# Kernel optimization log

Measured on AMD Instinct MI355X. Metric: run time of the kernel, lower is better.

Reference implementation:

```python
import jax, jax.numpy as jnp
import numpy as np

N_NODES = 100000


def _gcn_conv(x, src, dst, W, b, n):
    # PyG GCNConv: x' = D^-1/2 (A + I) D^-1/2 (x W) + b, edges flow src -> dst
    h = x @ W                                        # [n, out]
    ones = jnp.ones(src.shape[0], dtype=h.dtype)
    deg = jax.ops.segment_sum(ones, dst, num_segments=n) + 1.0  # +1 for self-loop
    dis = jax.lax.rsqrt(deg)                         # deg >= 1, no inf handling needed
    norm = dis[src] * dis[dst]                       # [E]
    agg = jax.ops.segment_sum(norm[:, None] * h[src], dst, num_segments=n)
    agg = agg + (dis * dis)[:, None] * h             # self-loop term, norm_ii = 1/deg_i
    return agg + b


def setup_inputs() -> dict:
    key = jax.random.key(0)
    k1, k2, k3, k4, k5, k6, k7, k8 = jax.random.split(key, 8)
    in_c, hid = 128, 64
    x = jax.random.normal(k1, (N_NODES, in_c), dtype=jnp.float32)
    edge_index = jax.random.randint(k2, (2, 1600000), 0, N_NODES, dtype=jnp.int64)
    s1 = 1.0 / np.sqrt(in_c)
    s2 = 1.0 / np.sqrt(hid)
    W1 = jax.random.uniform(k3, (in_c, hid), jnp.float32, -s1, s1)
    b1 = jnp.zeros((hid,), jnp.float32)
    W2 = jax.random.uniform(k4, (hid, hid), jnp.float32, -s2, s2)
    b2 = jnp.zeros((hid,), jnp.float32)
    Wl = jax.random.uniform(k5, (hid, 1), jnp.float32, -s2, s2)
    bl = jax.random.uniform(k6, (1,), jnp.float32, -s2, s2)
    return {"x": x, "edge_index": edge_index, "W1": W1, "b1": b1,
            "W2": W2, "b2": b2, "Wl": Wl, "bl": bl}


def reference(x, edge_index, W1, b1, W2, b2, Wl, bl):
    src, dst = edge_index[0], edge_index[1]
    n = x.shape[0]
    h = jax.nn.relu(_gcn_conv(x, src, dst, W1, b1, n))
    # dropout is identity in eval mode
    h = _gcn_conv(h, src, dst, W2, b2, n)
    return jax.nn.sigmoid(h @ Wl + bl)               # [n, 1]
```

## Files before the change

### kernel.cpp

```cpp
#include <hip/hip_runtime.h>
#include <hip/hip_bf16.h>


#define EPB 4096
#define NBMAX 512

typedef __attribute__((ext_vector_type(8))) short bf16x8;
typedef __attribute__((ext_vector_type(4))) float f32x4;

__device__ __forceinline__ unsigned short f2b(float f) {
    unsigned u = __builtin_bit_cast(unsigned, f);
    u += 0x7fffu + ((u >> 16) & 1u);
    return (unsigned short)(u >> 16);
}
__device__ __forceinline__ float b2f(unsigned short h) {
    unsigned u = (unsigned)h << 16;
    return __builtin_bit_cast(float, u);
}


__global__ __launch_bounds__(256) void bcount_k(
    const int* __restrict__ dst, int* __restrict__ bucket_cnt, int E, int nbuckets) {
    __shared__ int lh[NBMAX];
    int t = threadIdx.x;
    for (int i = t; i < nbuckets; i += 256) lh[i] = 0;
    __syncthreads();
    int e0 = blockIdx.x * EPB;
    int cnt = min(EPB, E - e0);
    for (int i = t; i < cnt; i += 256) atomicAdd(&lh[dst[e0 + i] >> 8], 1);
    __syncthreads();
    for (int i = t; i < nbuckets; i += 256)
        if (lh[i]) atomicAdd(&bucket_cnt[i], lh[i]);
}

__global__ __launch_bounds__(512) void bscan_k(
    const int* __restrict__ cnt, int* __restrict__ base, int* __restrict__ cur, int nb) {
    __shared__ int s[512];
    int t = threadIdx.x;
    int v = (t < nb) ? cnt[t] : 0;
    s[t] = v; __syncthreads();
    #pragma unroll
    for (int off = 1; off < 512; off <<= 1) {
        int u = (t >= off) ? s[t - off] : 0;
        __syncthreads();
        s[t] += u;
        __syncthreads();
    }
    if (t < nb) { int e = s[t] - v; base[t] = e; cur[t] = e; }
    if (t == nb - 1) base[nb] = s[t];
}

__global__ __launch_bounds__(256) void partition_k(
    const int* __restrict__ src, const int* __restrict__ dst,
    int* __restrict__ bucket_cur, int* __restrict__ stage, int E, int nbuckets) {
    __shared__ int ls[EPB];
    __shared__ int ld[EPB];
    __shared__ int lhist[NBMAX];
    __shared__ int lbase[NBMAX];
    int e0 = blockIdx.x * EPB;
    int cnt = min(EPB, E - e0);
    int t = threadIdx.x;
    for (int i = t; i < cnt; i += 256) { ls[i] = src[e0 + i]; ld[i] = dst[e0 + i]; }
    for (int b = t; b < nbuckets; b += 256) lhist[b] = 0;
    __syncthreads();
    for (int i = t; i < cnt; i += 256) atomicAdd(&lhist[ld[i] >> 8], 1);
    __syncthreads();
    for (int b = t; b < nbuckets; b += 256) {
        int c = lhist[b];
        lbase[b] = (c > 0) ? atomicAdd(&bucket_cur[b], c) : 0;
        lhist[b] = 0;
    }
    __syncthreads();
    for (int i = t; i < cnt; i += 256) {
        int d  = ld[i];
        int b  = d >> 8;
        int off = atomicAdd(&lhist[b], 1);
        stage[lbase[b] + off] = ls[i] | ((d & 255) << 17);
    }
}

__global__ __launch_bounds__(256) void bucket_place_k(
    const int* __restrict__ stage, const int* __restrict__ bucket_base,
    int* __restrict__ row_start, float* __restrict__ dis,
    int* __restrict__ csr_src, int n, int nbuckets) {
    __shared__ int lh[256];
    __shared__ int ss[256];
    __shared__ int lcur[256];
    int b = blockIdx.x;
    int t = threadIdx.x;
    int ebeg = bucket_base[b], eend = bucket_base[b + 1];
    int node0 = b << 8;

    lh[t] = 0;
    __syncthreads();
    for (int e = ebeg + t; e < eend; e += 256)
        atomicAdd(&lh[(stage[e] >> 17) & 255], 1);
    __syncthreads();

    int cnt = lh[t];
    ss[t] = cnt;
    __syncthreads();
    #pragma unroll
    for (int off = 1; off < 256; off <<= 1) {
        int u = (t >= off) ? ss[t - off] : 0;
        __syncthreads();
        ss[t] += u;
        __syncthreads();
    }
    int excl = ss[t] - cnt;
    int node = node0 + t;
    if (node < n) {
        row_start[node] = ebeg + excl;
        dis[node] = rsqrtf((float)cnt + 1.0f);
    }
    lcur[t] = ebeg + excl;
    if (b == nbuckets - 1 && t == 0) row_start[n] = eend;
    __syncthreads();

    for (int e = ebeg + t; e < eend; e += 256) {
        int p = stage[e];
        int pos = atomicAdd(&lcur[(p >> 17) & 255], 1);
        csr_src[pos] = p & 0x1FFFF;
    }
}

__global__ void wfrag_k(const float* __restrict__ W1, const float* __restrict__ W2,
                        unsigned short* __restrict__ fw1, float* __restrict__ w2l,
                        const float* __restrict__ b2, const float* __restrict__ Wl,
                        const float* __restrict__ bl, float* __restrict__ c0,
                        int* __restrict__ bcnt) {
    int gid = blockIdx.x * blockDim.x + threadIdx.x;
    if (gid <= NBMAX) bcnt[gid] = 0;
    if (blockIdx.x == 0 && threadIdx.x < 64) {
        float v = b2[threadIdx.x] * Wl[threadIdx.x];
        #pragma unroll
        for (int m = 32; m >= 1; m >>= 1) v += __shfl_xor(v, m);
        if (threadIdx.x == 0) c0[0] = v + bl[0];
    }
    if (blockIdx.x == 1 && threadIdx.x < 64) {
        int k = threadIdx.x;
        float s = 0.f;
        #pragma unroll 8
        for (int j = 0; j < 64; ++j) s = fmaf(W2[k * 64 + j], Wl[j], s);
        w2l[k] = s;
    }
    if (gid < 8192) {
        int f = gid >> 9, rem = gid & 511;
        int l = rem >> 3, i = rem & 7;
        int ks = f >> 2, ct = f & 3;
        int k = ks * 32 + ((l >> 4) << 3) + i;
        int c = ct * 16 + (l & 15);
        fw1[gid] = f2b(W1[k * 64 + c]);
    }
}

template <int K>
__global__ __launch_bounds__(256) void mfma_gemm_k(
    const float* __restrict__ X, const unsigned short* __restrict__ FW,
    const float* __restrict__ dis, unsigned short* __restrict__ Y, int n) {
    constexpr int KS = K / 32;
    int wave   = (int)((blockIdx.x * blockDim.x + threadIdx.x) >> 6);
    int lane   = threadIdx.x & 63;
    int nwaves = (int)((gridDim.x * blockDim.x) >> 6);
    int ntiles = n >> 4;

    bf16x8 bfrag[KS][4];
    #pragma unroll
    for (int ks = 0; ks < KS; ++ks)
        #pragma unroll
        for (int ct = 0; ct < 4; ++ct)
            bfrag[ks][ct] = *reinterpret_cast<const bf16x8*>(FW + ((ks * 4 + ct) << 9) + (lane << 3));

    int rb = lane & 15;
    int kb = (lane >> 4) << 3;

    for (int tile = wave; tile < ntiles; tile += nwaves) {
        int row = (tile << 4) + rb;
        f32x4 acc[4];
        #pragma unroll
        for (int ct = 0; ct < 4; ++ct) acc[ct] = (f32x4){0.f, 0.f, 0.f, 0.f};

        #pragma unroll
        for (int ks = 0; ks < KS; ++ks) {
            const float* p = X + (size_t)row * K + ks * 32 + kb;
            float4 u = *reinterpret_cast<const float4*>(p);
            float4 v = *reinterpret_cast<const float4*>(p + 4);
            bf16x8 af;
            af[0] = (short)f2b(u.x); af[1] = (short)f2b(u.y);
            af[2] = (short)f2b(u.z); af[3] = (short)f2b(u.w);
            af[4] = (short)f2b(v.x); af[5] = (short)f2b(v.y);
            af[6] = (short)f2b(v.z); af[7] = (short)f2b(v.w);
            #pragma unroll
            for (int ct = 0; ct < 4; ++ct)
                acc[ct] = __builtin_amdgcn_mfma_f32_16x16x32_bf16(af, bfrag[ks][ct], acc[ct], 0, 0, 0);
        }

        int orow0 = (tile << 4) + ((lane >> 4) << 2);
        int ocol  = lane & 15;
        float dv0 = dis[orow0], dv1 = dis[orow0 + 1], dv2 = dis[orow0 + 2], dv3 = dis[orow0 + 3];
        #pragma unroll
        for (int ct = 0; ct < 4; ++ct) {
            Y[(size_t)(orow0 + 0) * 64 + ct * 16 + ocol] = f2b(acc[ct][0] * dv0);
            Y[(size_t)(orow0 + 1) * 64 + ct * 16 + ocol] = f2b(acc[ct][1] * dv1);
            Y[(size_t)(orow0 + 2) * 64 + ct * 16 + ocol] = f2b(acc[ct][2] * dv2);
            Y[(size_t)(orow0 + 3) * 64 + ct * 16 + ocol] = f2b(acc[ct][3] * dv3);
        }
    }
}

__global__ __launch_bounds__(256) void gather_k(
    const int* __restrict__ row_start, const int* __restrict__ csr_src,
    const float* __restrict__ dis, const unsigned short* __restrict__ tp,
    const float* __restrict__ b, const float* __restrict__ w2l,
    float* __restrict__ z, int n) {
    int node = (int)((blockIdx.x * blockDim.x + threadIdx.x) >> 6);
    int lane = threadIdx.x & 63;
    if (node >= n) return;
    int beg = row_start[node], end = row_start[node + 1];
    float dd = dis[node];
    float a0 = b2f(tp[(size_t)node * 64 + lane]);
    float a1 = 0.f, a2 = 0.f, a3 = 0.f, a4 = 0.f, a5 = 0.f, a6 = 0.f, a7 = 0.f;

    for (int base = beg; base < end; base += 64) {
        int rem = end - base;
        int cnt = rem < 64 ? rem : 64;
        int idx = (lane < cnt) ? csr_src[base + lane] : 0;
        int j = 0;
        for (; j + 8 <= cnt; j += 8) {
            int s0 = __shfl(idx, j + 0), s1 = __shfl(idx, j + 1);
            int s2 = __shfl(idx, j + 2), s3 = __shfl(idx, j + 3);
            int s4 = __shfl(idx, j + 4), s5 = __shfl(idx, j + 5);
            int s6 = __shfl(idx, j + 6), s7 = __shfl(idx, j + 7);
            a0 += b2f(tp[(size_t)s0 * 64 + lane]);
            a1 += b2f(tp[(size_t)s1 * 64 + lane]);
            a2 += b2f(tp[(size_t)s2 * 64 + lane]);
            a3 += b2f(tp[(size_t)s3 * 64 + lane]);
            a4 += b2f(tp[(size_t)s4 * 64 + lane]);
            a5 += b2f(tp[(size_t)s5 * 64 + lane]);
            a6 += b2f(tp[(size_t)s6 * 64 + lane]);
            a7 += b2f(tp[(size_t)s7 * 64 + lane]);
        }
        if (j + 4 <= cnt) {
            int s0 = __shfl(idx, j + 0), s1 = __shfl(idx, j + 1);
            int s2 = __shfl(idx, j + 2), s3 = __shfl(idx, j + 3);
            a0 += b2f(tp[(size_t)s0 * 64 + lane]);
            a1 += b2f(tp[(size_t)s1 * 64 + lane]);
            a2 += b2f(tp[(size_t)s2 * 64 + lane]);
            a3 += b2f(tp[(size_t)s3 * 64 + lane]);
            j += 4;
        }
        for (; j < cnt; ++j) {
            int s = __shfl(idx, j);
            a4 += b2f(tp[(size_t)s * 64 + lane]);
        }
    }

    float acc = ((a0 + a1) + (a2 + a3)) + ((a4 + a5) + (a6 + a7));
    float h = fmaxf(fmaf(dd, acc, b[lane]), 0.f);
    float v = h * w2l[lane];
    #pragma unroll
    for (int m = 32; m >= 1; m >>= 1) v += __shfl_xor(v, m);
    if (lane == 0) z[node] = dd * v;
}

__global__ __launch_bounds__(256) void gatherz_k(
    const int* __restrict__ row_start, const int* __restrict__ csr_src,
    const float* __restrict__ dis, const float* __restrict__ z,
    const float* __restrict__ c0, float* __restrict__ out, int n) {
    int i = blockIdx.x * blockDim.x + threadIdx.x;
    if (i >= n) return;
    int beg = row_start[i], end = row_start[i + 1];
    float s0 = 0.f, s1 = 0.f, s2 = 0.f, s3 = 0.f;
    int e = beg;
    for (; e + 4 <= end; e += 4) {
        s0 += z[csr_src[e + 0]];
        s1 += z[csr_src[e + 1]];
        s2 += z[csr_src[e + 2]];
        s3 += z[csr_src[e + 3]];
    }
    for (; e < end; ++e) s0 += z[csr_src[e]];
    float v = fmaf(dis[i], z[i] + ((s0 + s1) + (s2 + s3)), c0[0]);
    out[i] = 1.f / (1.f + expf(-v));
}


__global__ void relu_k(float* __restrict__ p, long long m) {
    long long i = (long long)blockIdx.x * blockDim.x + threadIdx.x;
    if (i < m) p[i] = fmaxf(p[i], 0.f);
}
__global__ void deg_init_k(float* __restrict__ deg, int n) {
    int i = blockIdx.x * blockDim.x + threadIdx.x;
    if (i < n) deg[i] = 1.0f;
}
__global__ void deg_edges_k(const int* __restrict__ dst, float* __restrict__ deg, int E) {
    int e = blockIdx.x * blockDim.x + threadIdx.x;
    if (e < E) atomicAdd(&deg[dst[e]], 1.0f);
}
__global__ void dis_k(float* __restrict__ deg, int n) {
    int i = blockIdx.x * blockDim.x + threadIdx.x;
    if (i < n) deg[i] = rsqrtf(deg[i]);
}
__global__ void init_agg_k(const float* __restrict__ t, const float* __restrict__ dis,
                           const float* __restrict__ b, float* __restrict__ agg, int n) {
    int idx = blockIdx.x * blockDim.x + threadIdx.x;
    if (idx >= n * 64) return;
    int i = idx >> 6, jj = idx & 63;
    float ds = dis[i];
    agg[idx] = ds * ds * t[idx] + b[jj];
}
__global__ __launch_bounds__(256) void agg_edges_k(
    const int* __restrict__ src, const int* __restrict__ dst,
    const float* __restrict__ dis, const float* __restrict__ t,
    float* __restrict__ agg, int E) {
    int e    = (int)((blockIdx.x * blockDim.x + threadIdx.x) >> 6);
    int lane = threadIdx.x & 63;
    if (e >= E) return;
    int s = src[e], d = dst[e];
    float w = dis[s] * dis[d];
    atomicAdd(&agg[(size_t)d * 64 + lane], w * t[(size_t)s * 64 + lane]);
}
__global__ __launch_bounds__(256) void final_k(
    const float* __restrict__ agg, const float* __restrict__ Wl,
    const float* __restrict__ bl, float* __restrict__ out, int n) {
    int node = (int)((blockIdx.x * blockDim.x + threadIdx.x) >> 6);
    int lane = threadIdx.x & 63;
    if (node >= n) return;
    float v = agg[(size_t)node * 64 + lane] * Wl[lane];
    #pragma unroll
    for (int m = 32; m >= 1; m >>= 1) v += __shfl_xor(v, m);
    if (lane == 0) out[node] = 1.f / (1.f + expf(-(v + bl[0])));
}
template <int K>
__global__ __launch_bounds__(256) void gemm_rows4_k(
    const float* __restrict__ X, const float* __restrict__ W,
    float* __restrict__ Y, int n) {
    __shared__ float Ws[K * 64];
    for (int t = threadIdx.x; t < K * 64; t += blockDim.x) Ws[t] = W[t];
    __syncthreads();
    int wave   = (int)((blockIdx.x * blockDim.x + threadIdx.x) >> 6);
    int lane   = threadIdx.x & 63;
    int nwaves = (int)((gridDim.x * blockDim.x) >> 6);
    for (int r = wave; r < n; r += nwaves) {
        const float* xr = X + (size_t)r * K;
        float acc = 0.f;
        for (int k = 0; k < K; k += 4) {
            float4 a = *reinterpret_cast<const float4*>(xr + k);
            acc = fmaf(a.x, Ws[(k + 0) * 64 + lane], acc);
            acc = fmaf(a.y, Ws[(k + 1) * 64 + lane], acc);
            acc = fmaf(a.z, Ws[(k + 2) * 64 + lane], acc);
            acc = fmaf(a.w, Ws[(k + 3) * 64 + lane], acc);
        }
        Y[(size_t)r * 64 + lane] = acc;
    }
}


extern "C" void kernel_launch(void* const* d_in, const int* in_sizes, int n_in,
                              void* d_out, int out_size, void* d_ws, size_t ws_size,
                              hipStream_t stream) {
    const float* x  = (const float*)d_in[0];
    const int*   ei = (const int*)d_in[1];
    const float* W1 = (const float*)d_in[2];
    const float* b1 = (const float*)d_in[3];
    const float* W2 = (const float*)d_in[4];
    const float* b2 = (const float*)d_in[5];
    const float* Wl = (const float*)d_in[6];
    const float* bl = (const float*)d_in[7];
    float* out = (float*)d_out;

    const int n = in_sizes[0] / 128;
    const int E = in_sizes[1] / 2;
    const int* src = ei;
    const int* dst = ei + E;

    const int B = 256;
    dim3 blk(B);
    auto align512 = [](size_t v) { return (v + 511) & ~(size_t)511; };

    char* ws = (char*)d_ws;
    size_t off = 0;
    float*          dis     = (float*)(ws + off); off = align512(off + (size_t)n * 4);
    int*            row_st  = (int*)  (ws + off); off = align512(off + (size_t)(n + 1) * 4);
    int*            bcnt    = (int*)  (ws + off); off = align512(off + (size_t)(NBMAX + 1) * 4);
    int*            bbase   = (int*)  (ws + off); off = align512(off + (size_t)(NBMAX + 1) * 4);
    int*            bcur    = (int*)  (ws + off); off = align512(off + (size_t)NBMAX * 4);
    float*          c0      = (float*)(ws + off); off = align512(off + 512);
    float*          w2l     = (float*)(ws + off); off = align512(off + 64 * 4);
    float*          zbuf    = (float*)(ws + off); off = align512(off + (size_t)n * 4);
    int*            csr_src = (int*)  (ws + off); off = align512(off + (size_t)E * 4);
    unsigned short* bufA16  = (unsigned short*)(ws + off); off = align512(off + (size_t)n * 64 * 2);
    int*            stage   = (int*)  (ws + off); off = align512(off + (size_t)E * 4);
    unsigned short* fw1     = (unsigned short*)(ws + off); off = align512(off + 8192 * 2);
    size_t need_csr = off;

    const int nbuckets = (n + 255) >> 8;
    const int nebl = (E + EPB - 1) / EPB;

    if (ws_size >= need_csr && (n & 15) == 0 && nbuckets <= NBMAX && n <= (1 << 17)) {
        wfrag_k<<<48, blk, 0, stream>>>(W1, W2, fw1, w2l, b2, Wl, bl, c0, bcnt);

        bcount_k<<<nebl, blk, 0, stream>>>(dst, bcnt, E, nbuckets);
        bscan_k<<<1, 512, 0, stream>>>(bcnt, bbase, bcur, nbuckets);
        partition_k<<<nebl, blk, 0, stream>>>(src, dst, bcur, stage, E, nbuckets);
        bucket_place_k<<<nbuckets, blk, 0, stream>>>(stage, bbase, row_st, dis, csr_src, n, nbuckets);

        int gemm_blocks = ((n >> 4) + 3) / 4;

        mfma_gemm_k<128><<<gemm_blocks, blk, 0, stream>>>(x, fw1, dis, bufA16, n);

        gather_k<<<((size_t)n * 64 + B - 1) / B, blk, 0, stream>>>(
            row_st, csr_src, dis, bufA16, b1, w2l, zbuf, n);

        gatherz_k<<<(n + B - 1) / B, blk, 0, stream>>>(
            row_st, csr_src, dis, zbuf, c0, out, n);
    } else {
        size_t o2 = 0;
        float* dis2 = (float*)(ws + o2); o2 = align512(o2 + (size_t)n * 4);
        float* bA   = (float*)(ws + o2); o2 += (size_t)n * 64 * 4;
        float* bB   = (float*)(ws + o2);

        deg_init_k<<<(n + B - 1) / B, blk, 0, stream>>>(dis2, n);
        deg_edges_k<<<(E + B - 1) / B, blk, 0, stream>>>(dst, dis2, E);
        dis_k<<<(n + B - 1) / B, blk, 0, stream>>>(dis2, n);

        gemm_rows4_k<128><<<2048, blk, 0, stream>>>(x, W1, bA, n);
        init_agg_k<<<((size_t)n * 64 + B - 1) / B, blk, 0, stream>>>(bA, dis2, b1, bB, n);
        agg_edges_k<<<(E + 3) / 4, blk, 0, stream>>>(src, dst, dis2, bA, bB, E);
        relu_k<<<((size_t)n * 64 + B - 1) / B, blk, 0, stream>>>(bB, (long long)n * 64);

        gemm_rows4_k<64><<<2048, blk, 0, stream>>>(bB, W2, bA, n);
        init_agg_k<<<((size_t)n * 64 + B - 1) / B, blk, 0, stream>>>(bA, dis2, b2, bB, n);
        agg_edges_k<<<(E + 3) / 4, blk, 0, stream>>>(src, dst, dis2, bA, bB, E);

        final_k<<<(n + 3) / 4, blk, 0, stream>>>(bB, Wl, bl, out, n);
    }
}
```

Before: 132.6 us.

## Split gather features into four column-partitioned passes with per-pass partial sums

The GEMM now writes its bf16 output in four column-major slabs of 16 features, each of size n×16. The gather kernel launches four passes, one slab per pass, so each pass's working set is a quarter of the full feature table and is more likely to stay in cache. Within a wave, 8 edges are processed at once with each lane loading a 32-bit pair of features. Per-pass partial z values are written to a buffer and combined by a new zsum kernel. This adds an extra launch, four passes over the CSR index data, and cross-lane shuffle reductions.

```diff
diff --git a/kernel.cpp b/kernel.cpp
--- a/kernel.cpp
+++ b/kernel.cpp
@@ -16,6 +16,12 @@
 __device__ __forceinline__ float b2f(unsigned short h) {
     unsigned u = (unsigned)h << 16;
     return __builtin_bit_cast(float, u);
+}
+__device__ __forceinline__ float blo(unsigned u) {
+    return __builtin_bit_cast(float, u << 16);
+}
+__device__ __forceinline__ float bhi(unsigned u) {
+    return __builtin_bit_cast(float, u & 0xffff0000u);
 }
 
 
@@ -163,6 +169,7 @@
     int lane   = threadIdx.x & 63;
     int nwaves = (int)((gridDim.x * blockDim.x) >> 6);
     int ntiles = n >> 4;
+    size_t n16 = (size_t)n * 16;
 
     bf16x8 bfrag[KS][4];
     #pragma unroll
@@ -200,10 +207,11 @@
         float dv0 = dis[orow0], dv1 = dis[orow0 + 1], dv2 = dis[orow0 + 2], dv3 = dis[orow0 + 3];
         #pragma unroll
         for (int ct = 0; ct < 4; ++ct) {
-            Y[(size_t)(orow0 + 0) * 64 + ct * 16 + ocol] = f2b(acc[ct][0] * dv0);
-            Y[(size_t)(orow0 + 1) * 64 + ct * 16 + ocol] = f2b(acc[ct][1] * dv1);
-            Y[(size_t)(orow0 + 2) * 64 + ct * 16 + ocol] = f2b(acc[ct][2] * dv2);
-            Y[(size_t)(orow0 + 3) * 64 + ct * 16 + ocol] = f2b(acc[ct][3] * dv3);
+            unsigned short* yp = Y + (size_t)ct * n16 + (size_t)orow0 * 16 + ocol;
+            yp[0]  = f2b(acc[ct][0] * dv0);
+            yp[16] = f2b(acc[ct][1] * dv1);
+            yp[32] = f2b(acc[ct][2] * dv2);
+            yp[48] = f2b(acc[ct][3] * dv3);
         }
     }
 }
@@ -212,55 +220,53 @@
     const int* __restrict__ row_start, const int* __restrict__ csr_src,
     const float* __restrict__ dis, const unsigned short* __restrict__ tp,
     const float* __restrict__ b, const float* __restrict__ w2l,
-    float* __restrict__ z, int n) {
-    int node = (int)((blockIdx.x * blockDim.x + threadIdx.x) >> 6);
+    float* __restrict__ zpart, int n, int bpp) {
+    int blk  = blockIdx.x;
+    int pass = blk / bpp;
+    int node = ((blk % bpp) << 2) + (threadIdx.x >> 6);
     int lane = threadIdx.x & 63;
     if (node >= n) return;
+    int eo = lane >> 3;
+    int fh = lane & 7;
     int beg = row_start[node], end = row_start[node + 1];
     float dd = dis[node];
-    float a0 = b2f(tp[(size_t)node * 64 + lane]);
-    float a1 = 0.f, a2 = 0.f, a3 = 0.f, a4 = 0.f, a5 = 0.f, a6 = 0.f, a7 = 0.f;
+    const unsigned short* tpp = tp + (size_t)pass * n * 16;
+
+    float a0 = 0.f, a1 = 0.f;
+    if (eo == 0) {
+        unsigned u = *reinterpret_cast<const unsigned*>(tpp + (size_t)node * 16 + fh * 2);
+        a0 = blo(u); a1 = bhi(u);
+    }
 
     for (int base = beg; base < end; base += 64) {
         int rem = end - base;
         int cnt = rem < 64 ? rem : 64;
         int idx = (lane < cnt) ? csr_src[base + lane] : 0;
-        int j = 0;
-        for (; j + 8 <= cnt; j += 8) {
-            int s0 = __shfl(idx, j + 0), s1 = __shfl(idx, j + 1);
-            int s2 = __shfl(idx, j + 2), s3 = __shfl(idx, j + 3);
-            int s4 = __shfl(idx, j + 4), s5 = __shfl(idx, j + 5);
-            int s6 = __shfl(idx, j + 6), s7 = __shfl(idx, j + 7);
-            a0 += b2f(tp[(size_t)s0 * 64 + lane]);
-            a1 += b2f(tp[(size_t)s1 * 64 + lane]);
-            a2 += b2f(tp[(size_t)s2 * 64 + lane]);
-            a3 += b2f(tp[(size_t)s3 * 64 + lane]);
-            a4 += b2f(tp[(size_t)s4 * 64 + lane]);
-            a5 += b2f(tp[(size_t)s5 * 64 + lane]);
-            a6 += b2f(tp[(size_t)s6 * 64 + lane]);
-            a7 += b2f(tp[(size_t)s7 * 64 + lane]);
+        for (int j = 0; j < cnt; j += 8) {
+            int s = __shfl(idx, j + eo);
+            if (j + eo < cnt) {
+                unsigned u = *reinterpret_cast<const unsigned*>(tpp + (size_t)s * 16 + fh * 2);
+                a0 += blo(u); a1 += bhi(u);
+            }
         }
-        if (j + 4 <= cnt) {
-            int s0 = __shfl(idx, j + 0), s1 = __shfl(idx, j + 1);
-            int s2 = __shfl(idx, j + 2), s3 = __shfl(idx, j + 3);
-            a0 += b2f(tp[(size_t)s0 * 64 + lane]);
-            a1 += b2f(tp[(size_t)s1 * 64 + lane]);
-            a2 += b2f(tp[(size_t)s2 * 64 + lane]);
-            a3 += b2f(tp[(size_t)s3 * 64 + lane]);
-            j += 4;
-        }
-        for (; j < cnt; ++j) {
-            int s = __shfl(idx, j);
-            a4 += b2f(tp[(size_t)s * 64 + lane]);
-        }
-    }
-
-    float acc = ((a0 + a1) + (a2 + a3)) + ((a4 + a5) + (a6 + a7));
-    float h = fmaxf(fmaf(dd, acc, b[lane]), 0.f);
-    float v = h * w2l[lane];
-    #pragma unroll
-    for (int m = 32; m >= 1; m >>= 1) v += __shfl_xor(v, m);
-    if (lane == 0) z[node] = dd * v;
+    }
+
+    a0 += __shfl_xor(a0, 8);  a1 += __shfl_xor(a1, 8);
+    a0 += __shfl_xor(a0, 16); a1 += __shfl_xor(a1, 16);
+    a0 += __shfl_xor(a0, 32); a1 += __shfl_xor(a1, 32);
+
+    int f0 = (pass << 4) + (fh << 1);
+    float h0 = fmaxf(fmaf(dd, a0, b[f0]), 0.f);
+    float h1 = fmaxf(fmaf(dd, a1, b[f0 + 1]), 0.f);
+    float v = fmaf(h0, w2l[f0], h1 * w2l[f0 + 1]);
+    v += __shfl_xor(v, 1); v += __shfl_xor(v, 2); v += __shfl_xor(v, 4);
+    if (lane == 0) zpart[(size_t)pass * n + node] = dd * v;
+}
+
+__global__ void zsum_k(const float* __restrict__ zp, float* __restrict__ z, int n) {
+    int i = blockIdx.x * blockDim.x + threadIdx.x;
+    if (i < n)
+        z[i] = (zp[i] + zp[(size_t)n + i]) + (zp[2 * (size_t)n + i] + zp[3 * (size_t)n + i]);
 }
 
 __global__ __launch_bounds__(256) void gatherz_k(
@@ -386,6 +392,7 @@
     int*            bcur    = (int*)  (ws + off); off = align512(off + (size_t)NBMAX * 4);
     float*          c0      = (float*)(ws + off); off = align512(off + 512);
     float*          w2l     = (float*)(ws + off); off = align512(off + 64 * 4);
+    float*          zpart   = (float*)(ws + off); off = align512(off + (size_t)n * 4 * 4);
     float*          zbuf    = (float*)(ws + off); off = align512(off + (size_t)n * 4);
     int*            csr_src = (int*)  (ws + off); off = align512(off + (size_t)E * 4);
     unsigned short* bufA16  = (unsigned short*)(ws + off); off = align512(off + (size_t)n * 64 * 2);
@@ -408,8 +415,10 @@
 
         mfma_gemm_k<128><<<gemm_blocks, blk, 0, stream>>>(x, fw1, dis, bufA16, n);
 
-        gather_k<<<((size_t)n * 64 + B - 1) / B, blk, 0, stream>>>(
-            row_st, csr_src, dis, bufA16, b1, w2l, zbuf, n);
+        int bpp = (n + 3) >> 2;
+        gather_k<<<4 * bpp, blk, 0, stream>>>(
+            row_st, csr_src, dis, bufA16, b1, w2l, zpart, n, bpp);
+        zsum_k<<<(n + B - 1) / B, blk, 0, stream>>>(zpart, zbuf, n);
 
         gatherz_k<<<(n + B - 1) / B, blk, 0, stream>>>(
             row_st, csr_src, dis, zbuf, c0, out, n);
```

Measured after the change: 214.7 us. +61.9%, slower.

## Drop bucket count/scan passes using fixed-capacity bucket staging; unroll gather by 16

Applied to the files above, without the earlier changes.

Removes the separate bucket-count and scan kernels by giving each destination bucket a fixed-capacity slot in the staging buffer. Partition atomically claims offsets within each bucket's slot, and bucket_place computes its global base by summing the counts of earlier buckets. The gather loop also issues 16 neighbor loads per iteration to raise memory-level parallelism. The risk is correctness: a bucket with more edges than the capacity (average plus 1024) overflows its slot, so skewed graphs would give wrong results.

```diff
diff --git a/kernel.cpp b/kernel.cpp
--- a/kernel.cpp
+++ b/kernel.cpp
@@ -19,40 +19,10 @@
 }
 
 
-__global__ __launch_bounds__(256) void bcount_k(
-    const int* __restrict__ dst, int* __restrict__ bucket_cnt, int E, int nbuckets) {
-    __shared__ int lh[NBMAX];
-    int t = threadIdx.x;
-    for (int i = t; i < nbuckets; i += 256) lh[i] = 0;
-    __syncthreads();
-    int e0 = blockIdx.x * EPB;
-    int cnt = min(EPB, E - e0);
-    for (int i = t; i < cnt; i += 256) atomicAdd(&lh[dst[e0 + i] >> 8], 1);
-    __syncthreads();
-    for (int i = t; i < nbuckets; i += 256)
-        if (lh[i]) atomicAdd(&bucket_cnt[i], lh[i]);
-}
-
-__global__ __launch_bounds__(512) void bscan_k(
-    const int* __restrict__ cnt, int* __restrict__ base, int* __restrict__ cur, int nb) {
-    __shared__ int s[512];
-    int t = threadIdx.x;
-    int v = (t < nb) ? cnt[t] : 0;
-    s[t] = v; __syncthreads();
-    #pragma unroll
-    for (int off = 1; off < 512; off <<= 1) {
-        int u = (t >= off) ? s[t - off] : 0;
-        __syncthreads();
-        s[t] += u;
-        __syncthreads();
-    }
-    if (t < nb) { int e = s[t] - v; base[t] = e; cur[t] = e; }
-    if (t == nb - 1) base[nb] = s[t];
-}
-
 __global__ __launch_bounds__(256) void partition_k(
     const int* __restrict__ src, const int* __restrict__ dst,
-    int* __restrict__ bucket_cur, int* __restrict__ stage, int E, int nbuckets) {
+    int* __restrict__ bucket_cur, int* __restrict__ stage,
+    int E, int nbuckets, int cap) {
     __shared__ int ls[EPB];
     __shared__ int ld[EPB];
     __shared__ int lhist[NBMAX];
@@ -75,25 +45,37 @@
         int d  = ld[i];
         int b  = d >> 8;
         int off = atomicAdd(&lhist[b], 1);
-        stage[lbase[b] + off] = ls[i] | ((d & 255) << 17);
+        stage[(size_t)b * cap + lbase[b] + off] = ls[i] | ((d & 255) << 17);
     }
 }
 
 __global__ __launch_bounds__(256) void bucket_place_k(
-    const int* __restrict__ stage, const int* __restrict__ bucket_base,
+    const int* __restrict__ stage, const int* __restrict__ bucket_cnt,
     int* __restrict__ row_start, float* __restrict__ dis,
-    int* __restrict__ csr_src, int n, int nbuckets) {
+    int* __restrict__ csr_src, int n, int nbuckets, int cap) {
+    __shared__ int red[256];
     __shared__ int lh[256];
     __shared__ int ss[256];
     __shared__ int lcur[256];
     int b = blockIdx.x;
     int t = threadIdx.x;
-    int ebeg = bucket_base[b], eend = bucket_base[b + 1];
-    int node0 = b << 8;
+    int total = bucket_cnt[b];
+
+    int partial = 0;
+    for (int i = t; i < b; i += 256) partial += bucket_cnt[i];
+    red[t] = partial; __syncthreads();
+    #pragma unroll
+    for (int m = 128; m > 0; m >>= 1) {
+        if (t < m) red[t] += red[t + m];
+        __syncthreads();
+    }
+    int base = red[0];
 
     lh[t] = 0;
     __syncthreads();
-    for (int e = ebeg + t; e < eend; e += 256)
+    size_t ebeg = (size_t)b * cap;
+    size_t eend = ebeg + total;
+    for (size_t e = ebeg + t; e < eend; e += 256)
         atomicAdd(&lh[(stage[e] >> 17) & 255], 1);
     __syncthreads();
 
@@ -108,16 +90,16 @@
         __syncthreads();
     }
     int excl = ss[t] - cnt;
-    int node = node0 + t;
+    int node = (b << 8) + t;
     if (node < n) {
-        row_start[node] = ebeg + excl;
+        row_start[node] = base + excl;
         dis[node] = rsqrtf((float)cnt + 1.0f);
     }
-    lcur[t] = ebeg + excl;
-    if (b == nbuckets - 1 && t == 0) row_start[n] = eend;
-    __syncthreads();
-
-    for (int e = ebeg + t; e < eend; e += 256) {
+    lcur[t] = base + excl;
+    if (b == nbuckets - 1 && t == 0) row_start[n] = base + total;
+    __syncthreads();
+
+    for (size_t e = ebeg + t; e < eend; e += 256) {
         int p = stage[e];
         int pos = atomicAdd(&lcur[(p >> 17) & 255], 1);
         csr_src[pos] = p & 0x1FFFF;
@@ -128,9 +110,9 @@
                         unsigned short* __restrict__ fw1, float* __restrict__ w2l,
                         const float* __restrict__ b2, const float* __restrict__ Wl,
                         const float* __restrict__ bl, float* __restrict__ c0,
-                        int* __restrict__ bcnt) {
+                        int* __restrict__ bcur) {
     int gid = blockIdx.x * blockDim.x + threadIdx.x;
-    if (gid <= NBMAX) bcnt[gid] = 0;
+    if (gid < NBMAX) bcur[gid] = 0;
     if (blockIdx.x == 0 && threadIdx.x < 64) {
         float v = b2[threadIdx.x] * Wl[threadIdx.x];
         #pragma unroll
@@ -226,7 +208,19 @@
         int cnt = rem < 64 ? rem : 64;
         int idx = (lane < cnt) ? csr_src[base + lane] : 0;
         int j = 0;
-        for (; j + 8 <= cnt; j += 8) {
+        for (; j + 16 <= cnt; j += 16) {
+            int   sarr[16];
+            float varr[16];
+            #pragma unroll
+            for (int k = 0; k < 16; ++k) sarr[k] = __shfl(idx, j + k);
+            #pragma unroll
+            for (int k = 0; k < 16; ++k) varr[k] = b2f(tp[(size_t)sarr[k] * 64 + lane]);
+            a0 += varr[0];  a1 += varr[1];  a2 += varr[2];  a3 += varr[3];
+            a4 += varr[4];  a5 += varr[5];  a6 += varr[6];  a7 += varr[7];
+            a0 += varr[8];  a1 += varr[9];  a2 += varr[10]; a3 += varr[11];
+            a4 += varr[12]; a5 += varr[13]; a6 += varr[14]; a7 += varr[15];
+        }
+        if (j + 8 <= cnt) {
             int s0 = __shfl(idx, j + 0), s1 = __shfl(idx, j + 1);
             int s2 = __shfl(idx, j + 2), s3 = __shfl(idx, j + 3);
             int s4 = __shfl(idx, j + 4), s5 = __shfl(idx, j + 5);
@@ -239,6 +233,7 @@
             a5 += b2f(tp[(size_t)s5 * 64 + lane]);
             a6 += b2f(tp[(size_t)s6 * 64 + lane]);
             a7 += b2f(tp[(size_t)s7 * 64 + lane]);
+            j += 8;
         }
         if (j + 4 <= cnt) {
             int s0 = __shfl(idx, j + 0), s1 = __shfl(idx, j + 1);
@@ -377,32 +372,30 @@
     dim3 blk(B);
     auto align512 = [](size_t v) { return (v + 511) & ~(size_t)511; };
 
+    const int nbuckets = (n + 255) >> 8;
+    const int CAP = nbuckets > 0 ? (((E / nbuckets) + 1024 + 63) & ~63) : 0;
+
     char* ws = (char*)d_ws;
     size_t off = 0;
     float*          dis     = (float*)(ws + off); off = align512(off + (size_t)n * 4);
     int*            row_st  = (int*)  (ws + off); off = align512(off + (size_t)(n + 1) * 4);
-    int*            bcnt    = (int*)  (ws + off); off = align512(off + (size_t)(NBMAX + 1) * 4);
-    int*            bbase   = (int*)  (ws + off); off = align512(off + (size_t)(NBMAX + 1) * 4);
     int*            bcur    = (int*)  (ws + off); off = align512(off + (size_t)NBMAX * 4);
     float*          c0      = (float*)(ws + off); off = align512(off + 512);
     float*          w2l     = (float*)(ws + off); off = align512(off + 64 * 4);
     float*          zbuf    = (float*)(ws + off); off = align512(off + (size_t)n * 4);
     int*            csr_src = (int*)  (ws + off); off = align512(off + (size_t)E * 4);
     unsigned short* bufA16  = (unsigned short*)(ws + off); off = align512(off + (size_t)n * 64 * 2);
-    int*            stage   = (int*)  (ws + off); off = align512(off + (size_t)E * 4);
+    int*            stage   = (int*)  (ws + off); off = align512(off + (size_t)nbuckets * CAP * 4);
     unsigned short* fw1     = (unsigned short*)(ws + off); off = align512(off + 8192 * 2);
     size_t need_csr = off;
 
-    const int nbuckets = (n + 255) >> 8;
     const int nebl = (E + EPB - 1) / EPB;
 
     if (ws_size >= need_csr && (n & 15) == 0 && nbuckets <= NBMAX && n <= (1 << 17)) {
-        wfrag_k<<<48, blk, 0, stream>>>(W1, W2, fw1, w2l, b2, Wl, bl, c0, bcnt);
-
-        bcount_k<<<nebl, blk, 0, stream>>>(dst, bcnt, E, nbuckets);
-        bscan_k<<<1, 512, 0, stream>>>(bcnt, bbase, bcur, nbuckets);
-        partition_k<<<nebl, blk, 0, stream>>>(src, dst, bcur, stage, E, nbuckets);
-        bucket_place_k<<<nbuckets, blk, 0, stream>>>(stage, bbase, row_st, dis, csr_src, n, nbuckets);
+        wfrag_k<<<48, blk, 0, stream>>>(W1, W2, fw1, w2l, b2, Wl, bl, c0, bcur);
+
+        partition_k<<<nebl, blk, 0, stream>>>(src, dst, bcur, stage, E, nbuckets, CAP);
+        bucket_place_k<<<nbuckets, blk, 0, stream>>>(stage, bcur, row_st, dis, csr_src, n, nbuckets, CAP);
 
         int gemm_blocks = ((n >> 4) + 3) / 4;
 
```

Result: faster. 122.2 us (-7.9%).
